# Performance work log

Hardware: AMD Instinct MI355X
Metric: run time of the kernel (lower is better)

Reference implementation:

```python
import jax, jax.numpy as jnp
import numpy as np

N, E = 100000, 1600000
DIM, H, D = 64, 4, 8          # dim, num_heads, qk_dim
DH = D * H                    # 32
QK_SCALE = (DIM // H) ** -0.5


def setup_inputs() -> dict:
    key = jax.random.key(0)
    k1, k2, k3, k4 = jax.random.split(key, 4)
    x = jax.random.normal(k1, (N, DIM), dtype=jnp.float32)
    edge_index = jax.random.randint(k2, (2, E), 0, N, dtype=jnp.int64)
    W_qkv = jax.random.normal(k3, (DIM, 2 * DH + DIM), dtype=jnp.float32) * (DIM ** -0.5)
    b_qkv = jax.random.normal(k4, (2 * DH + DIM,), dtype=jnp.float32) * 0.02
    return {"x": x, "edge_index": edge_index, "W_qkv": W_qkv, "b_qkv": b_qkv}


def reference(x, edge_index, W_qkv, b_qkv):
    n = x.shape[0]
    e = edge_index.shape[1]
    qkv = x @ W_qkv + b_qkv                       # (N, 2*DH+DIM)
    q = qkv[:, :DH].reshape(n, H, D)
    k = qkv[:, DH:2 * DH].reshape(n, H, D)
    v = qkv[:, 2 * DH:].reshape(n, H, DIM // H)
    s, t = edge_index[0], edge_index[1]
    q_e = q[s] * QK_SCALE                         # (E, H, D)
    k_e = k[t]
    v_e = v[t]                                    # (E, H, DIM/H)
    # scale q by 1/sqrt(num source neighbors) (bincount of s)
    deg = jax.ops.segment_sum(jnp.ones((e,), x.dtype), s, num_segments=n)
    q_e = q_e * (deg[s] ** -0.5)[:, None, None]
    compat = jnp.einsum('ehd,ehd->eh', q_e, k_e)  # (E, H)
    # segment softmax over edges grouped by source node s
    m = jax.ops.segment_max(compat, s, num_segments=n)
    ex = jnp.exp(compat - m[s])
    denom = jax.ops.segment_sum(ex, s, num_segments=n)
    attn = ex / (denom[s] + 1e-16)                # (E, H)
    msg = (v_e * attn[..., None]).reshape(e, DIM)  # (E, DIM)
    out = jax.ops.segment_sum(msg, s, num_segments=n)  # (N, DIM)
    return out
```

## Files before the change

kernel.cpp:

```cpp
#include <hip/hip_runtime.h>


#define NDIM 64
#define NBMAX 1024
#define CTILE 8192
#define STGMAX 4352
#define GEMM_BLKS 256

static __device__ __forceinline__ unsigned short f2bf(float f) {
    unsigned int u = __float_as_uint(f);
    unsigned int r = (u + 0x7fffu + ((u >> 16) & 1u)) >> 16;
    return (unsigned short)r;
}
static __device__ __forceinline__ float bflo(unsigned int u) {
    return __uint_as_float(u << 16);
}
static __device__ __forceinline__ float bfhi(unsigned int u) {
    return __uint_as_float(u & 0xffff0000u);
}

__global__ void fused_bin_gemm_kernel(const int* __restrict__ s_arr,
                                      const int* __restrict__ t_arr,
                                      unsigned int* __restrict__ gcur,
                                      unsigned int* __restrict__ binned,
                                      const float* __restrict__ x,
                                      const float* __restrict__ W,
                                      const float* __restrict__ bvec,
                                      unsigned short* __restrict__ qs16,
                                      unsigned short* __restrict__ kv,
                                      int N, int E, int nbin) {
    __shared__ unsigned int sm[12288];
    unsigned int* hist  = sm;
    unsigned int* off   = sm + 1024;
    unsigned int* gbase = sm + 2048;
    unsigned int* psum  = sm + 3072;
    unsigned int* stg   = sm + 4096;
    int tid = threadIdx.x;

    if (blockIdx.x < (unsigned)nbin) {
        int e0 = blockIdx.x * CTILE;
        int cnt = min(CTILE, E - e0);

        hist[tid] = 0;
        __syncthreads();
        for (int i = tid; i < cnt; i += 1024)
            atomicAdd(&hist[(unsigned)s_arr[e0 + i] >> 7], 1u);
        __syncthreads();

        unsigned int v = hist[tid];
        unsigned int acc = v;
        psum[tid] = acc;
        __syncthreads();
        for (int o = 1; o < 1024; o <<= 1) {
            unsigned int add = (tid >= o) ? psum[tid - o] : 0;
            __syncthreads();
            acc += add;
            psum[tid] = acc;
            __syncthreads();
        }
        off[tid] = acc - v;
        __syncthreads();

        for (int i = tid; i < cnt; i += 1024) {
            int s = s_arr[e0 + i];
            int t = t_arr[e0 + i];
            unsigned int bkt = (unsigned)s >> 7;
            unsigned int p = atomicAdd(&off[bkt], 1u);
            stg[p] = ((unsigned)(s & 127) << 17) | (unsigned)t;
        }
        __syncthreads();

        {
            unsigned int h = hist[tid];
            unsigned int resv = h ? atomicAdd(&gcur[tid], h) : 0u;
            unsigned int m = (resv < STGMAX) ? min(h, STGMAX - resv) : 0u;
            hist[tid] = m;
            gbase[tid] = (unsigned)tid * STGMAX + resv;
        }
        __syncthreads();

        int wid = tid >> 6, lane = tid & 63;
        for (int b = wid; b < NBMAX; b += 16) {
            unsigned int m = hist[b];
            if (m == 0) continue;
            unsigned int start = (b > 0) ? psum[b - 1] : 0u;
            unsigned int dst = gbase[b];
            for (unsigned int i = lane; i < m; i += 64)
                binned[dst + i] = stg[start + i];
        }
    } else {
        float4* xs = (float4*)sm;
        int bid = blockIdx.x - nbin;
        int col = tid & 127;
        int rw  = tid >> 7;
        float w[64];
        #pragma unroll
        for (int k = 0; k < 64; ++k) w[k] = W[k * 128 + col];
        float bias = bvec[col];

        for (int r0 = bid * 8; r0 < N; r0 += GEMM_BLKS * 8) {
            __syncthreads();
            if (tid < 128) {
                int rr = tid >> 4;
                int cc = tid & 15;
                int n = r0 + rr;
                xs[rr * 16 + cc] = (n < N)
                    ? reinterpret_cast<const float4*>(x)[(size_t)n * 16 + cc]
                    : make_float4(0.f, 0.f, 0.f, 0.f);
            }
            __syncthreads();
            int n = r0 + rw;
            if (n < N) {
                float acc = bias;
                #pragma unroll
                for (int k4 = 0; k4 < 16; ++k4) {
                    float4 xv = xs[rw * 16 + k4];
                    acc = fmaf(xv.x, w[4 * k4 + 0], acc);
                    acc = fmaf(xv.y, w[4 * k4 + 1], acc);
                    acc = fmaf(xv.z, w[4 * k4 + 2], acc);
                    acc = fmaf(xv.w, w[4 * k4 + 3], acc);
                }
                if (col < 32) {
                    qs16[(size_t)n * 32 + col] = f2bf(acc);
                } else if (col < 64) {
                    kv[(size_t)n * 96 + (col - 32)] = f2bf(acc);
                } else {
                    kv[(size_t)n * 96 + 32 + (col - 64)] = f2bf(acc);
                }
            }
        }
    }
}

__global__ void __launch_bounds__(512, 8)
sort_aggregate_kernel(const unsigned int* __restrict__ gcur,
                      const unsigned int* __restrict__ binned,
                      const unsigned short* __restrict__ qs16,
                      const unsigned int* __restrict__ kv32,
                      float* __restrict__ out, int N) {
    __shared__ unsigned int hist[128];
    __shared__ unsigned int rstart[128];
    __shared__ unsigned int cur[128];
    __shared__ unsigned int sh[128];
    __shared__ unsigned int stg[STGMAX];

    int b = blockIdx.x;
    int tid = threadIdx.x;
    unsigned int base = (unsigned)b * STGMAX;
    unsigned int cnt = min(gcur[b], (unsigned int)STGMAX);

    if (tid < 128) hist[tid] = 0;
    __syncthreads();
    for (unsigned int i = tid; i < cnt; i += 512)
        atomicAdd(&hist[binned[base + i] >> 17], 1u);
    __syncthreads();

    unsigned int v = (tid < 128) ? hist[tid] : 0;
    unsigned int acc = v;
    if (tid < 128) sh[tid] = acc;
    __syncthreads();
    for (int o = 1; o < 128; o <<= 1) {
        unsigned int add = (tid >= o && tid < 128) ? sh[tid - o] : 0;
        __syncthreads();
        if (tid < 128) { acc += add; sh[tid] = acc; }
        __syncthreads();
    }
    if (tid < 128) {
        unsigned int exc = acc - v;
        rstart[tid] = exc;
        cur[tid] = exc;
    }
    __syncthreads();

    for (unsigned int i = tid; i < cnt; i += 512) {
        unsigned int e = binned[base + i];
        unsigned int p = atomicAdd(&cur[e >> 17], 1u);
        stg[p] = (e & 0x1FFFFu) * 192u;
    }
    __syncthreads();

    int wid = tid >> 6, lane = tid & 63;
    int hl   = lane & 31;
    int sub  = lane >> 5;
    int head = hl >> 3;
    const char* kvb = (const char*)kv32;
    const char* qsb = (const char*)qs16;

    for (int nl = wid * 16; nl < wid * 16 + 16; ++nl) {
        int n = b * 128 + nl;
        if (n >= N) break;
        int dg = (int)hist[nl];
        if (dg == 0) {
            if (lane < 32)
                *reinterpret_cast<float2*>(&out[(size_t)n * 64 + 2 * hl]) =
                    make_float2(0.f, 0.f);
            continue;
        }
        int start = (int)rstart[nl];
        int last = start + dg - 1;
        float sc = 0.25f * rsqrtf((float)dg);

        uint4 q4 = *(const uint4*)(qsb + (size_t)n * 64 + (head << 4));
        float qf0 = bflo(q4.x) * sc, qf1 = bfhi(q4.x) * sc;
        float qf2 = bflo(q4.y) * sc, qf3 = bfhi(q4.y) * sc;
        float qf4 = bflo(q4.z) * sc, qf5 = bfhi(q4.z) * sc;
        float qf6 = bflo(q4.w) * sc, qf7 = bfhi(q4.w) * sc;

        float accx = 0.f, accy = 0.f, den = 0.f;
        int npairs = (dg + 1) >> 1;
        int idx = start + sub;

        unsigned int co = stg[min(idx, last)];
        float wm = (idx <= last) ? 1.f : 0.f;
        uint4 kr = *(const uint4*)(kvb + co + (head << 4));
        unsigned int vr = *(const unsigned int*)(kvb + co + 64 + (hl << 2));

        for (int i = 0; i < npairs; ++i) {
            uint4 kr2 = kr; unsigned int vr2 = vr; float wm2 = 0.f;
            int idx2 = idx + 2;
            if (i + 1 < npairs) {
                unsigned int co2 = stg[min(idx2, last)];
                wm2 = (idx2 <= last) ? 1.f : 0.f;
                kr2 = *(const uint4*)(kvb + co2 + (head << 4));
                vr2 = *(const unsigned int*)(kvb + co2 + 64 + (hl << 2));
            }
            float p = qf0 * bflo(kr.x);
            p = fmaf(qf1, bfhi(kr.x), p);
            p = fmaf(qf2, bflo(kr.y), p);
            p = fmaf(qf3, bfhi(kr.y), p);
            p = fmaf(qf4, bflo(kr.z), p);
            p = fmaf(qf5, bfhi(kr.z), p);
            p = fmaf(qf6, bflo(kr.w), p);
            p = fmaf(qf7, bfhi(kr.w), p);
            float w = __expf(p) * wm;
            accx = fmaf(w, bflo(vr), accx);
            accy = fmaf(w, bfhi(vr), accy);
            den += w;
            kr = kr2; vr = vr2; wm = wm2; idx = idx2;
        }

        accx += __shfl_xor(accx, 32);
        accy += __shfl_xor(accy, 32);
        den  += __shfl_xor(den, 32);

        if (lane < 32) {
            float inv = 1.0f / (den + 1e-16f);
            *reinterpret_cast<float2*>(&out[(size_t)n * 64 + 2 * hl]) =
                make_float2(accx * inv, accy * inv);
        }
    }
}

extern "C" void kernel_launch(void* const* d_in, const int* in_sizes, int n_in,
                              void* d_out, int out_size, void* d_ws, size_t ws_size,
                              hipStream_t stream) {
    const float* x = (const float*)d_in[0];
    const int*   eidx = (const int*)d_in[1];
    const float* W = (const float*)d_in[2];
    const float* b = (const float*)d_in[3];
    int N = in_sizes[0] / NDIM;
    int E = in_sizes[1] / 2;
    float* out = (float*)d_out;

    int NB = (N + 127) / 128;
    int nbin = (E + CTILE - 1) / CTILE;

    unsigned short* qs16 = (unsigned short*)d_ws;
    unsigned short* kv = qs16 + (size_t)N * 32;
    unsigned int* gcur = (unsigned int*)(kv + (size_t)N * 96);
    unsigned int* binned = gcur + NBMAX;

    const int* s_arr = eidx;
    const int* t_arr = eidx + E;

    hipMemsetAsync(gcur, 0, NBMAX * sizeof(unsigned int), stream);

    fused_bin_gemm_kernel<<<nbin + GEMM_BLKS, 1024, 0, stream>>>(
        s_arr, t_arr, gcur, binned, x, W, b, qs16, kv, N, E, nbin);
    sort_aggregate_kernel<<<NB, 512, 0, stream>>>(
        gcur, binned, qs16, (const unsigned int*)kv, out, N);
}
```

Baseline: 171.5 us.

## Scatter binned edges directly to global memory, dropping LDS staging and scan

The binning blocks no longer build a block-local prefix scan and stage the packed edges in shared memory before copying them out per bucket. Each block now reserves global space per bucket right after the histogram, and every thread takes a slot with a shared-memory atomic and writes its packed edge straight to global memory. Shared memory per block drops from 48KB to 8KB, which may let more blocks share a CU, and the GEMM block count is raised. In exchange the global writes are scattered and uncoalesced instead of contiguous per bucket, and the order of edges inside a bucket becomes nondeterministic.

```diff
diff --git a/kernel.cpp b/kernel.cpp
--- a/kernel.cpp
+++ b/kernel.cpp
@@ -5,7 +5,7 @@
 #define NBMAX 1024
 #define CTILE 8192
 #define STGMAX 4352
-#define GEMM_BLKS 256
+#define GEMM_BLKS 316
 
 static __device__ __forceinline__ unsigned short f2bf(float f) {
     unsigned int u = __float_as_uint(f);
@@ -29,15 +29,12 @@
                                       unsigned short* __restrict__ qs16,
                                       unsigned short* __restrict__ kv,
                                       int N, int E, int nbin) {
-    __shared__ unsigned int sm[12288];
-    unsigned int* hist  = sm;
-    unsigned int* off   = sm + 1024;
-    unsigned int* gbase = sm + 2048;
-    unsigned int* psum  = sm + 3072;
-    unsigned int* stg   = sm + 4096;
+    __shared__ unsigned int sm[2048];
     int tid = threadIdx.x;
 
     if (blockIdx.x < (unsigned)nbin) {
+        unsigned int* hist  = sm;
+        unsigned int* gbase = sm + 1024;
         int e0 = blockIdx.x * CTILE;
         int cnt = min(CTILE, E - e0);
 
@@ -46,47 +43,20 @@
         for (int i = tid; i < cnt; i += 1024)
             atomicAdd(&hist[(unsigned)s_arr[e0 + i] >> 7], 1u);
         __syncthreads();
-
-        unsigned int v = hist[tid];
-        unsigned int acc = v;
-        psum[tid] = acc;
-        __syncthreads();
-        for (int o = 1; o < 1024; o <<= 1) {
-            unsigned int add = (tid >= o) ? psum[tid - o] : 0;
-            __syncthreads();
-            acc += add;
-            psum[tid] = acc;
-            __syncthreads();
-        }
-        off[tid] = acc - v;
-        __syncthreads();
-
+        {
+            unsigned int h = hist[tid];
+            gbase[tid] = h
+                ? (unsigned)tid * STGMAX + atomicAdd(&gcur[tid], h)
+                : 0u;
+        }
+        __syncthreads();
         for (int i = tid; i < cnt; i += 1024) {
             int s = s_arr[e0 + i];
             int t = t_arr[e0 + i];
             unsigned int bkt = (unsigned)s >> 7;
-            unsigned int p = atomicAdd(&off[bkt], 1u);
-            stg[p] = ((unsigned)(s & 127) << 17) | (unsigned)t;
-        }
-        __syncthreads();
-
-        {
-            unsigned int h = hist[tid];
-            unsigned int resv = h ? atomicAdd(&gcur[tid], h) : 0u;
-            unsigned int m = (resv < STGMAX) ? min(h, STGMAX - resv) : 0u;
-            hist[tid] = m;
-            gbase[tid] = (unsigned)tid * STGMAX + resv;
-        }
-        __syncthreads();
-
-        int wid = tid >> 6, lane = tid & 63;
-        for (int b = wid; b < NBMAX; b += 16) {
-            unsigned int m = hist[b];
-            if (m == 0) continue;
-            unsigned int start = (b > 0) ? psum[b - 1] : 0u;
-            unsigned int dst = gbase[b];
-            for (unsigned int i = lane; i < m; i += 64)
-                binned[dst + i] = stg[start + i];
+            unsigned int dst = atomicAdd(&gbase[bkt], 1u);
+            if (dst < (bkt + 1u) * STGMAX)
+                binned[dst] = ((unsigned)(s & 127) << 17) | (unsigned)t;
         }
     } else {
         float4* xs = (float4*)sm;
```

Result: slower. 183.8 us (+7.2%).
